# Optimization experiments

Measured on AMD Instinct MI355X. Metric: run time of the kernel, lower is better.

## Reference

```python
import jax, jax.numpy as jnp
import numpy as np

H = 1024   # x-axis resolution
W = 1024   # y-axis resolution
HID = 256  # hidden_size (image setting per paper)
C = 3      # RGB out_channels


def _siren_uniform(key, shape, fan_in):
    b = np.sqrt(6.0 / fan_in)
    return jax.random.uniform(key, shape, minval=-b, maxval=b, dtype=jnp.float32)


def setup_inputs() -> dict:
    key = jax.random.key(0)
    ks = jax.random.split(key, 16)
    x = jax.random.uniform(ks[0], (H, 1), minval=-1.0, maxval=1.0, dtype=jnp.float32)
    y = jax.random.uniform(ks[1], (W, 1), minval=-1.0, maxval=1.0, dtype=jnp.float32)
    return {
        "x": x, "y": y,
        # per-axis branch Linear(1, HID)
        "bw0": _siren_uniform(ks[2], (HID, 1), 1), "bb0": _siren_uniform(ks[3], (HID,), 1),
        "bw1": _siren_uniform(ks[4], (HID, 1), 1), "bb1": _siren_uniform(ks[5], (HID,), 1),
        # shared premerge: Sine -> Linear -> Sine -> Linear -> Sine
        "pw1": _siren_uniform(ks[6], (HID, HID), HID), "pb1": _siren_uniform(ks[7], (HID,), HID),
        "pw2": _siren_uniform(ks[8], (HID, HID), HID), "pb2": _siren_uniform(ks[9], (HID,), HID),
        # postmerge: Linear -> Sine -> Linear -> Sigmoid
        "qw1": _siren_uniform(ks[10], (HID, HID), HID), "qb1": _siren_uniform(ks[11], (HID,), HID),
        "qw2": _siren_uniform(ks[12], (C, HID), HID), "qb2": _siren_uniform(ks[13], (C,), HID),
    }


def reference(x, y, bw0, bb0, bw1, bb1, pw1, pb1, pw2, pb2, qw1, qb1, qw2, qb2):
    def premerge(h):
        # Sine(w0=1) -> Linear -> Sine -> Linear -> Sine
        h = jnp.sin(h)
        h = jnp.sin(h @ pw1.T + pb1)
        h = jnp.sin(h @ pw2.T + pb2)
        return h

    fx = premerge(x @ bw0.T + bb0)  # [H, HID]
    fy = premerge(y @ bw1.T + bb1)  # [W, HID]
    merged = jnp.einsum('ik,jk->ijk', fx, fy)          # [H, W, HID] outer-product fusion
    h = jnp.sin(merged @ qw1.T + qb1)                  # [H, W, HID]
    out = jax.nn.sigmoid(h @ qw2.T + qb2)              # [H, W, C]
    return jnp.transpose(out, (2, 1, 0))               # [C, W, H]
```

## Files before the change

kernel.cpp:

```cpp
#include <hip/hip_runtime.h>

#define HH  1024
#define WW  1024
#define HID 256

typedef __attribute__((ext_vector_type(4))) float f32x4;
typedef __attribute__((ext_vector_type(8))) short short8;

static __device__ __forceinline__ unsigned short f2bf(float x) {
    unsigned u = __builtin_bit_cast(unsigned, x);
    u = (u + 0x7fffu + ((u >> 16) & 1u)) >> 16;
    return (unsigned short)u;
}


__global__ __launch_bounds__(256) void transpose_k(
    const float* __restrict__ pw1, const float* __restrict__ pw2,
    float* __restrict__ pw1t, float* __restrict__ pw2t)
{
    __shared__ float tile[32][33];
    const float* src = blockIdx.z ? pw2 : pw1;
    float*       dst = blockIdx.z ? pw2t : pw1t;
    const int bx = blockIdx.x * 32, by = blockIdx.y * 32;
    const int tx = threadIdx.x & 31, ty0 = threadIdx.x >> 5;
    #pragma unroll
    for (int r = 0; r < 32; r += 8)
        tile[ty0 + r][tx] = src[(by + ty0 + r) * HID + bx + tx];
    __syncthreads();
    #pragma unroll
    for (int r = 0; r < 32; r += 8)
        dst[(bx + ty0 + r) * HID + by + tx] = tile[tx][ty0 + r];
}

__global__ __launch_bounds__(256) void branch_k(
    const float* __restrict__ x, const float* __restrict__ y,
    const float* __restrict__ bw0, const float* __restrict__ bb0,
    const float* __restrict__ bw1, const float* __restrict__ bb1,
    float* __restrict__ s0)
{
    const int t  = threadIdx.x;
    const int g0 = blockIdx.x * 8;
    const int axis = g0 >> 10;
    const float* coord = axis ? y : x;
    const float* bw = axis ? bw1 : bw0;
    const float* bb = axis ? bb1 : bb0;
    const int base = g0 & 1023;
    const float wv = bw[t], bv = bb[t];
    #pragma unroll
    for (int q = 0; q < 8; ++q)
        s0[(g0 + q) * HID + t] = __sinf(coord[base + q] * wv + bv);
}

__global__ __launch_bounds__(256) void layer_k(
    const float* __restrict__ sin_in,
    const float* __restrict__ wt,
    const float* __restrict__ bias,
    float* __restrict__ sout,
    unsigned short* __restrict__ fxT, float* __restrict__ fy_f,
    const int is_final)
{
    const int t  = threadIdx.x;
    const int g0 = blockIdx.x * 8;
    float acc[8];
    const float bv = bias[t];
    #pragma unroll
    for (int q = 0; q < 8; ++q) acc[q] = bv;
    const float* srow = sin_in + g0 * HID;
    for (int c = 0; c < HID; ++c) {
        const float wv = wt[c * HID + t];
        #pragma unroll
        for (int q = 0; q < 8; ++q) acc[q] += srow[q * HID + c] * wv;
    }
    if (!is_final) {
        #pragma unroll
        for (int q = 0; q < 8; ++q) sout[(g0 + q) * HID + t] = __sinf(acc[q]);
    } else {
        const int f  = ((t >> 7) << 2) | ((t >> 5) & 3);
        const int lg = (t >> 3) & 3, e = t & 7;
        #pragma unroll
        for (int q = 0; q < 8; ++q) {
            const float h = __sinf(acc[q]);
            const int g = g0 + q;
            if (g < HH) {
                const int ti = g >> 4, il = g & 15;
                fxT[ti * 4096 + f * 512 + (lg * 16 + il) * 8 + e] = f2bf(h);
            } else {
                fy_f[(g - HH) * HID + t] = h;
            }
        }
    }
}

__global__ __launch_bounds__(256, 2) void fused_k(
    const float* __restrict__ qw1, const float* __restrict__ qb1,
    const float* __restrict__ qw2, const float* __restrict__ qb2,
    const unsigned short* __restrict__ fxT, const float* __restrict__ fy_f,
    float* __restrict__ out)
{
    const int j   = blockIdx.x;
    const int tid = threadIdx.x;
    const int l   = tid & 63;
    const int w   = tid >> 6;
    const int n0  = w * 64;
    const int il  = l & 15;
    const int lg  = l >> 4;

    float qb1r[4][4], qw2r[3][4][4];
    #pragma unroll
    for (int nt = 0; nt < 4; ++nt) {
        #pragma unroll
        for (int r = 0; r < 4; ++r) {
            const int n = n0 + nt * 16 + lg * 4 + r;
            qb1r[nt][r]    = qb1[n];
            qw2r[0][nt][r] = qw2[0 * HID + n];
            qw2r[1][nt][r] = qw2[1 * HID + n];
            qw2r[2][nt][r] = qw2[2 * HID + n];
        }
    }
    const float qb2v0 = qb2[0], qb2v1 = qb2[1], qb2v2 = qb2[2];

    short8 afrag[4][8];
    #pragma unroll
    for (int kt = 0; kt < 8; ++kt) {
        const int kb = kt * 32 + lg * 8;
        const f32x4 fA = *(const f32x4*)&fy_f[j * HID + kb];
        const f32x4 fB = *(const f32x4*)&fy_f[j * HID + kb + 4];
        #pragma unroll
        for (int nt = 0; nt < 4; ++nt) {
            const int n = n0 + nt * 16 + il;
            const f32x4 qA = *(const f32x4*)&qw1[n * HID + kb];
            const f32x4 qB = *(const f32x4*)&qw1[n * HID + kb + 4];
            short8 f;
            f[0] = (short)f2bf(qA[0] * fA[0]);
            f[1] = (short)f2bf(qA[1] * fA[1]);
            f[2] = (short)f2bf(qA[2] * fA[2]);
            f[3] = (short)f2bf(qA[3] * fA[3]);
            f[4] = (short)f2bf(qB[0] * fB[0]);
            f[5] = (short)f2bf(qB[1] * fB[1]);
            f[6] = (short)f2bf(qB[2] * fB[2]);
            f[7] = (short)f2bf(qB[3] * fB[3]);
            afrag[nt][kt] = f;
        }
    }

    __shared__ __attribute__((aligned(16))) char tile[3][8192];
    __shared__ float red[4][3][256];

    const char* fxb = (const char*)fxT;
    const unsigned off0 = (unsigned)((w * 2 + 0) * 1024 + l * 16);
    const unsigned off1 = (unsigned)((w * 2 + 1) * 1024 + l * 16);

#define STAGE(slot, tidx)                                                        \
    do {                                                                         \
        const char* _src = fxb + (unsigned)(tidx) * 8192u;                       \
        __builtin_amdgcn_global_load_lds(                                        \
            (const __attribute__((address_space(1))) unsigned*)(_src + off0),    \
            (__attribute__((address_space(3))) unsigned*)(&tile[slot][off0]),    \
            16, 0, 0);                                                           \
        __builtin_amdgcn_global_load_lds(                                        \
            (const __attribute__((address_space(1))) unsigned*)(_src + off1),    \
            (__attribute__((address_space(3))) unsigned*)(&tile[slot][off1]),    \
            16, 0, 0);                                                           \
    } while (0)

#define WAITBAR asm volatile("s_waitcnt vmcnt(2) lgkmcnt(0)\n\ts_barrier" ::: "memory")

    STAGE(0, 0);
    STAGE(1, 1);
    WAITBAR;

    int itg = 0;
    int cur = 0;
    for (int seg = 0; seg < 4; ++seg) {
        for (int it16 = 0; it16 < 16; ++it16, ++itg) {
            {
                int s2 = cur + 2; if (s2 >= 3) s2 -= 3;
                const int tidx = (itg + 2) & 63;
                switch (s2) {
                    case 0: STAGE(0, tidx); break;
                    case 1: STAGE(1, tidx); break;
                    default: STAGE(2, tidx); break;
                }
            }
            f32x4 acc[4];
            #pragma unroll
            for (int nt = 0; nt < 4; ++nt) {
                acc[nt][0] = qb1r[nt][0]; acc[nt][1] = qb1r[nt][1];
                acc[nt][2] = qb1r[nt][2]; acc[nt][3] = qb1r[nt][3];
            }
            const char* tb = &tile[cur][l * 16];
            #pragma unroll
            for (int f = 0; f < 8; ++f) {
                const short8 bfrag = *(const short8*)(tb + f * 1024);
                #pragma unroll
                for (int nt = 0; nt < 4; ++nt)
                    acc[nt] = __builtin_amdgcn_mfma_f32_16x16x32_bf16(
                        afrag[nt][f], bfrag, acc[nt], 0, 0, 0);
            }
            float p0 = 0.f, p1 = 0.f, p2 = 0.f;
            #pragma unroll
            for (int nt = 0; nt < 4; ++nt) {
                #pragma unroll
                for (int r = 0; r < 4; ++r) {
                    const float s = __sinf(acc[nt][r]);
                    p0 += qw2r[0][nt][r] * s;
                    p1 += qw2r[1][nt][r] * s;
                    p2 += qw2r[2][nt][r] * s;
                }
            }
            p0 += __shfl_xor(p0, 16); p0 += __shfl_xor(p0, 32);
            p1 += __shfl_xor(p1, 16); p1 += __shfl_xor(p1, 32);
            p2 += __shfl_xor(p2, 16); p2 += __shfl_xor(p2, 32);
            if (l < 16) {
                const int ic = it16 * 16 + l;
                red[w][0][ic] = p0;
                red[w][1][ic] = p1;
                red[w][2][ic] = p2;
            }
            WAITBAR;
            cur = cur + 1 == 3 ? 0 : cur + 1;
        }
        {
            const int ib = j * HH + seg * 256 + tid;
            #pragma unroll
            for (int q = 0; q < 3; ++q) {
                const float v = red[0][q][tid] + red[1][q][tid]
                              + red[2][q][tid] + red[3][q][tid]
                              + (q == 0 ? qb2v0 : (q == 1 ? qb2v1 : qb2v2));
                out[q * (WW * HH) + ib] = 1.0f / (1.0f + __expf(-v));
            }
        }
        asm volatile("s_waitcnt lgkmcnt(0)\n\ts_barrier" ::: "memory");
    }
#undef STAGE
#undef WAITBAR
}

extern "C" void kernel_launch(void* const* d_in, const int* in_sizes, int n_in,
                              void* d_out, int out_size, void* d_ws, size_t ws_size,
                              hipStream_t stream)
{
    const float* x   = (const float*)d_in[0];
    const float* y   = (const float*)d_in[1];
    const float* bw0 = (const float*)d_in[2];
    const float* bb0 = (const float*)d_in[3];
    const float* bw1 = (const float*)d_in[4];
    const float* bb1 = (const float*)d_in[5];
    const float* pw1 = (const float*)d_in[6];
    const float* pb1 = (const float*)d_in[7];
    const float* pw2 = (const float*)d_in[8];
    const float* pb2 = (const float*)d_in[9];
    const float* qw1 = (const float*)d_in[10];
    const float* qb1 = (const float*)d_in[11];
    const float* qw2 = (const float*)d_in[12];
    const float* qb2 = (const float*)d_in[13];

    char* ws = (char*)d_ws;
    unsigned short* fxT = (unsigned short*)(ws);
    float* fy_f = (float*)(ws + (512 << 10));
    float* pw1t = (float*)(ws + (1536 << 10));
    float* pw2t = (float*)(ws + (1792 << 10));
    float* s0   = (float*)(ws + (2048 << 10));
    float* s1   = (float*)(ws + (4096 << 10));
    float* out  = (float*)d_out;

    transpose_k<<<dim3(8, 8, 2), 256, 0, stream>>>(pw1, pw2, pw1t, pw2t);
    branch_k<<<256, 256, 0, stream>>>(x, y, bw0, bb0, bw1, bb1, s0);
    layer_k<<<256, 256, 0, stream>>>(s0, pw1t, pb1, s1, nullptr, nullptr, 0);
    layer_k<<<256, 256, 0, stream>>>(s1, pw2t, pb2, nullptr, fxT, fy_f, 1);
    fused_k<<<WW, 256, 0, stream>>>(qw1, qb1, qw2, qb2, fxT, fy_f, out);
}
```

Before: 234.2 us.

## Double-buffer two fused tiles per stage and halve barrier count

Replaces the triple-buffered 8KB tile ring with a double-buffered 16KB ring, where each stage loads two tiles. Each stage runs two independent MFMA accumulator chains with batched LDS fragment loads, then two sine/projection epilogues. The intent is one barrier per two tiles instead of one per tile, plus more instruction-level parallelism from the interleaved accumulators. The risk is that the wait on outstanding loads sits after the barrier, so another wave's LDS writes may not be complete before the next tile is read, and the deeper fused epilogue raises register pressure.

```diff
diff --git a/kernel.cpp b/kernel.cpp
--- a/kernel.cpp
+++ b/kernel.cpp
@@ -143,16 +143,16 @@
         }
     }
 
-    __shared__ __attribute__((aligned(16))) char tile[3][8192];
+    __shared__ __attribute__((aligned(16))) char tile[2][16384];
     __shared__ float red[4][3][256];
 
     const char* fxb = (const char*)fxT;
     const unsigned off0 = (unsigned)((w * 2 + 0) * 1024 + l * 16);
     const unsigned off1 = (unsigned)((w * 2 + 1) * 1024 + l * 16);
 
-#define STAGE(slot, tidx)                                                        \
+#define STAGE2(slot, sidx)                                                       \
     do {                                                                         \
-        const char* _src = fxb + (unsigned)(tidx) * 8192u;                       \
+        const char* _src = fxb + (unsigned)(sidx) * 16384u;                      \
         __builtin_amdgcn_global_load_lds(                                        \
             (const __attribute__((address_space(1))) unsigned*)(_src + off0),    \
             (__attribute__((address_space(3))) unsigned*)(&tile[slot][off0]),    \
@@ -161,66 +161,85 @@
             (const __attribute__((address_space(1))) unsigned*)(_src + off1),    \
             (__attribute__((address_space(3))) unsigned*)(&tile[slot][off1]),    \
             16, 0, 0);                                                           \
+        __builtin_amdgcn_global_load_lds(                                        \
+            (const __attribute__((address_space(1))) unsigned*)(_src + 8192 + off0), \
+            (__attribute__((address_space(3))) unsigned*)(&tile[slot][8192 + off0]), \
+            16, 0, 0);                                                           \
+        __builtin_amdgcn_global_load_lds(                                        \
+            (const __attribute__((address_space(1))) unsigned*)(_src + 8192 + off1), \
+            (__attribute__((address_space(3))) unsigned*)(&tile[slot][8192 + off1]), \
+            16, 0, 0);                                                           \
     } while (0)
 
-#define WAITBAR asm volatile("s_waitcnt vmcnt(2) lgkmcnt(0)\n\ts_barrier" ::: "memory")
-
-    STAGE(0, 0);
-    STAGE(1, 1);
-    WAITBAR;
-
-    int itg = 0;
+#define TILE_MFMA(accv, tbase)                                                   \
+    do {                                                                         \
+        _Pragma("unroll")                                                        \
+        for (int g = 0; g < 2; ++g) {                                            \
+            short8 bf[4];                                                        \
+            _Pragma("unroll")                                                    \
+            for (int kk = 0; kk < 4; ++kk)                                       \
+                bf[kk] = *(const short8*)((tbase) + (g * 4 + kk) * 1024);        \
+            _Pragma("unroll")                                                    \
+            for (int kk = 0; kk < 4; ++kk) {                                     \
+                _Pragma("unroll")                                                \
+                for (int nt = 0; nt < 4; ++nt)                                   \
+                    accv[nt] = __builtin_amdgcn_mfma_f32_16x16x32_bf16(          \
+                        afrag[nt][g * 4 + kk], bf[kk], accv[nt], 0, 0, 0);       \
+            }                                                                    \
+        }                                                                        \
+    } while (0)
+
+#define EPILOGUE(accv, t16)                                                      \
+    do {                                                                         \
+        float p0 = 0.f, p1 = 0.f, p2 = 0.f;                                      \
+        _Pragma("unroll")                                                        \
+        for (int nt = 0; nt < 4; ++nt) {                                         \
+            _Pragma("unroll")                                                    \
+            for (int r = 0; r < 4; ++r) {                                        \
+                const float s = __sinf(accv[nt][r]);                             \
+                p0 += qw2r[0][nt][r] * s;                                        \
+                p1 += qw2r[1][nt][r] * s;                                        \
+                p2 += qw2r[2][nt][r] * s;                                        \
+            }                                                                    \
+        }                                                                        \
+        p0 += __shfl_xor(p0, 16); p0 += __shfl_xor(p0, 32);                      \
+        p1 += __shfl_xor(p1, 16); p1 += __shfl_xor(p1, 32);                      \
+        p2 += __shfl_xor(p2, 16); p2 += __shfl_xor(p2, 32);                      \
+        if (l < 16) {                                                            \
+            const int ic = (t16) * 16 + l;                                       \
+            red[w][0][ic] = p0;                                                  \
+            red[w][1][ic] = p1;                                                  \
+            red[w][2][ic] = p2;                                                  \
+        }                                                                        \
+    } while (0)
+
+    STAGE2(0, 0);
+    STAGE2(1, 1);
+    asm volatile("s_waitcnt vmcnt(4)" ::: "memory");
+    asm volatile("s_barrier" ::: "memory");
+
     int cur = 0;
-    for (int seg = 0; seg < 4; ++seg) {
-        for (int it16 = 0; it16 < 16; ++it16, ++itg) {
-            {
-                int s2 = cur + 2; if (s2 >= 3) s2 -= 3;
-                const int tidx = (itg + 2) & 63;
-                switch (s2) {
-                    case 0: STAGE(0, tidx); break;
-                    case 1: STAGE(1, tidx); break;
-                    default: STAGE(2, tidx); break;
-                }
-            }
-            f32x4 acc[4];
-            #pragma unroll
-            for (int nt = 0; nt < 4; ++nt) {
-                acc[nt][0] = qb1r[nt][0]; acc[nt][1] = qb1r[nt][1];
-                acc[nt][2] = qb1r[nt][2]; acc[nt][3] = qb1r[nt][3];
-            }
-            const char* tb = &tile[cur][l * 16];
-            #pragma unroll
-            for (int f = 0; f < 8; ++f) {
-                const short8 bfrag = *(const short8*)(tb + f * 1024);
-                #pragma unroll
-                for (int nt = 0; nt < 4; ++nt)
-                    acc[nt] = __builtin_amdgcn_mfma_f32_16x16x32_bf16(
-                        afrag[nt][f], bfrag, acc[nt], 0, 0, 0);
-            }
-            float p0 = 0.f, p1 = 0.f, p2 = 0.f;
-            #pragma unroll
-            for (int nt = 0; nt < 4; ++nt) {
-                #pragma unroll
-                for (int r = 0; r < 4; ++r) {
-                    const float s = __sinf(acc[nt][r]);
-                    p0 += qw2r[0][nt][r] * s;
-                    p1 += qw2r[1][nt][r] * s;
-                    p2 += qw2r[2][nt][r] * s;
-                }
-            }
-            p0 += __shfl_xor(p0, 16); p0 += __shfl_xor(p0, 32);
-            p1 += __shfl_xor(p1, 16); p1 += __shfl_xor(p1, 32);
-            p2 += __shfl_xor(p2, 16); p2 += __shfl_xor(p2, 32);
-            if (l < 16) {
-                const int ic = it16 * 16 + l;
-                red[w][0][ic] = p0;
-                red[w][1][ic] = p1;
-                red[w][2][ic] = p2;
-            }
-            WAITBAR;
-            cur = cur + 1 == 3 ? 0 : cur + 1;
-        }
-        {
+    for (int ss = 0; ss < 32; ++ss) {
+        f32x4 accA[4], accB[4];
+        #pragma unroll
+        for (int nt = 0; nt < 4; ++nt) {
+            accA[nt][0] = qb1r[nt][0]; accA[nt][1] = qb1r[nt][1];
+            accA[nt][2] = qb1r[nt][2]; accA[nt][3] = qb1r[nt][3];
+            accB[nt][0] = qb1r[nt][0]; accB[nt][1] = qb1r[nt][1];
+            accB[nt][2] = qb1r[nt][2]; accB[nt][3] = qb1r[nt][3];
+        }
+        const char* tbA = &tile[cur][l * 16];
+        const char* tbB = &tile[cur][8192 + l * 16];
+        TILE_MFMA(accA, tbA);
+        TILE_MFMA(accB, tbB);
+        const int t16 = 2 * (ss & 7);
+        EPILOGUE(accA, t16);
+        EPILOGUE(accB, t16 + 1);
+
+        const int sidx = (ss + 2) & 31;
+        if ((ss & 7) == 7) {
+            asm volatile("s_waitcnt lgkmcnt(0)\n\ts_barrier" ::: "memory");
+            const int seg = ss >> 3;
             const int ib = j * HH + seg * 256 + tid;
             #pragma unroll
             for (int q = 0; q < 3; ++q) {
@@ -229,11 +248,19 @@
                               + (q == 0 ? qb2v0 : (q == 1 ? qb2v1 : qb2v2));
                 out[q * (WW * HH) + ib] = 1.0f / (1.0f + __expf(-v));
             }
-        }
-        asm volatile("s_waitcnt lgkmcnt(0)\n\ts_barrier" ::: "memory");
-    }
-#undef STAGE
-#undef WAITBAR
+            asm volatile("s_barrier" ::: "memory");
+            if (cur == 0) STAGE2(0, sidx); else STAGE2(1, sidx);
+            asm volatile("s_waitcnt vmcnt(7)" ::: "memory");
+        } else {
+            asm volatile("s_barrier" ::: "memory");
+            if (cur == 0) STAGE2(0, sidx); else STAGE2(1, sidx);
+            asm volatile("s_waitcnt vmcnt(4)" ::: "memory");
+        }
+        cur ^= 1;
+    }
+#undef STAGE2
+#undef TILE_MFMA
+#undef EPILOGUE
 }
 
 extern "C" void kernel_launch(void* const* d_in, const int* in_sizes, int n_in,
```

New measurement: 231.4 us. No clear change (-1.2%).
